# Performance work log

Hardware: AMD Instinct MI355X
Metric: run time of the kernel (lower is better)

The kernel has to match this reference:

```python
import jax, jax.numpy as jnp
import numpy as np

H = 4  # num_heads (hard-coded in module)
RATION = 5


def setup_inputs() -> dict:
    key = jax.random.key(0)
    ks = jax.random.split(key, 14)
    B, T, S, F = 256, 5, 64, 256
    u = 0.05  # keras 'uniform' initializer scale
    d = {}
    d["x"] = jax.random.normal(ks[0], (B, T, S, F), jnp.float32)
    d["atten_bias"] = jax.random.uniform(ks[1], (B, T, S, S), jnp.float32) * 0.1
    d["W_q"] = jax.random.uniform(ks[2], (F, F), jnp.float32, -u, u)
    d["W_v"] = jax.random.uniform(ks[3], (F, F), jnp.float32, -u, u)
    d["W_o"] = jax.random.uniform(ks[4], (F, F), jnp.float32, -u, u)
    d["u_t"] = jax.random.uniform(ks[5], (T,), jnp.float32, -u, u)
    d["dis"] = jax.random.uniform(ks[6], (T, S, S), jnp.float32, -u, u)
    # keep sigma away from 0 to avoid blowing up the Gaussian prior
    d["sigma"] = jax.random.uniform(ks[7], (T, S, 1), jnp.float32, 0.5, 1.0)
    # SE block: fc1 Dense(T*RATION, relu, he_normal), fc2 Dense(T, sigmoid)
    d["fc1_w"] = jax.random.normal(ks[8], (T, T * RATION), jnp.float32) * np.sqrt(2.0 / T).astype(np.float32)
    d["fc1_b"] = jnp.zeros((T * RATION,), jnp.float32)
    d["fc2_w"] = jax.random.normal(ks[9], (T * RATION, T), jnp.float32) * np.sqrt(2.0 / (T * RATION)).astype(np.float32)
    d["fc2_b"] = jnp.zeros((T,), jnp.float32)
    d["bili_w"] = jax.random.uniform(ks[10], (1,), jnp.float32, -u, u)
    return d


def _se_block(o, fc1_w, fc1_b, fc2_w, fc2_b, bili_w):
    # o: [B,T,S,F] -> transpose to [B,S,F,T]; "channel" axis is T
    xt = jnp.transpose(o, (0, 2, 3, 1))
    avg = jnp.mean(xt, axis=(1, 2))  # [B,T]
    mx = jnp.max(xt, axis=(1, 2))    # [B,T]
    se1 = jax.nn.sigmoid(jax.nn.relu(avg @ fc1_w + fc1_b) @ fc2_w + fc2_b)
    se2 = jax.nn.sigmoid(jax.nn.relu(mx @ fc1_w + fc1_b) @ fc2_w + fc2_b)
    w = bili_w  # shape (1,)
    se = (1.0 - w) * se1 + w * se2   # [B,T]
    out = xt * se[:, None, None, :]
    return jnp.transpose(out, (0, 3, 1, 2))  # back to [B,T,S,F]


def reference(x, atten_bias, W_q, W_v, W_o, u_t, dis, sigma, fc1_w, fc1_b, fc2_w, fc2_b, bili_w):
    B, T, S, F = x.shape
    Fh = F // H
    # q, v: project then reshape (row-major split, exactly as TF reshape)
    q = (x @ W_q).reshape(-1, T, S, Fh)          # [H*B, T, S, Fh]
    v = (x @ W_v).reshape(-1, T, S, Fh)          # [H*B, T, S, Fh]
    # k: contract time with u_t, then [B,F,S] -> [H*B, Fh, S]
    k = jnp.einsum('t,btsf->bsf', u_t, x)        # [B, S, F]
    k = jnp.transpose(k, (0, 2, 1)).reshape(-1, Fh, S)  # [H*B, Fh, S]
    score = jnp.einsum('btsf,bfc->btsc', q, k) / jnp.sqrt(jnp.asarray(Fh, x.dtype))
    score = jax.nn.sigmoid(score)                # [H*B, T, S, S]
    score = score - jnp.tile(atten_bias, (H, 1, 1, 1))
    # learned spatial Gaussian prior, broadcast over batch
    prior = (1.0 / (jnp.sqrt(2.0 * jnp.pi) * sigma)) * jnp.exp(-dis ** 2 / (2.0 * sigma ** 2))
    score = score * prior
    # Dropout(0.3) is identity at inference
    score = jnp.sum(score, axis=-2)              # [H*B, T, S]
    atten = v * score[..., None]                 # [H*B, T, S, Fh]
    o = atten.reshape(-1, T, S, F) @ W_o         # [B, T, S, F]
    o = _se_block(o, fc1_w, fc1_b, fc2_w, fc2_b, bili_w)
    return o + x
```

## Files before the change

### kernel.cpp

```cpp
#include <hip/hip_runtime.h>


typedef unsigned short ushort_t;
typedef __attribute__((ext_vector_type(8))) short bf16x8;
typedef __attribute__((ext_vector_type(4))) float f32x4;

__device__ inline ushort_t f2bf(float f) {
  unsigned u = __float_as_uint(f);
  return (ushort_t)((u + 0x7FFFu + ((u >> 16) & 1u)) >> 16);
}
__device__ inline float bflo(unsigned u) { return __uint_as_float(u << 16); }
__device__ inline float bfhi(unsigned u) { return __uint_as_float(u & 0xFFFF0000u); }
__device__ inline uint4 pack8(float4 a, float4 b) {
  uint4 r;
  r.x = (unsigned)f2bf(a.x) | ((unsigned)f2bf(a.y) << 16);
  r.y = (unsigned)f2bf(a.z) | ((unsigned)f2bf(a.w) << 16);
  r.z = (unsigned)f2bf(b.x) | ((unsigned)f2bf(b.y) << 16);
  r.w = (unsigned)f2bf(b.z) | ((unsigned)f2bf(b.w) << 16);
  return r;
}
__device__ inline void gload16(const ushort_t* g, ushort_t* l) {
  __builtin_amdgcn_global_load_lds((const __attribute__((address_space(1))) void*)g,
                                   (__attribute__((address_space(3))) void*)l, 16, 0, 0);
}

__global__ __launch_bounds__(256, 4) void prep_kernel(
    const float* __restrict__ x, const float* __restrict__ u,
    const float* __restrict__ Wq, const float* __restrict__ Wv,
    const float* __restrict__ Wo, const float* __restrict__ dis,
    const float* __restrict__ sigma, const float* __restrict__ bias,
    ushort_t* __restrict__ Wt, float* __restrict__ prior,
    float* __restrict__ bps, ushort_t* __restrict__ kout,
    ushort_t* __restrict__ xb) {
  __shared__ float red[4][64];
  const int blk = blockIdx.x, tid = threadIdx.x;
  if (blk < 768) {
    int id = blk * 256 + tid;
    int mat = id >> 16, rem = id & 65535;
    int n = rem >> 8, k = rem & 255;
    const float* W = mat == 0 ? Wq : (mat == 1 ? Wv : Wo);
    Wt[id] = f2bf(W[k * 256 + n]);
  } else if (blk < 848) {
    int i = (blk - 768) * 256 + tid;
    int ts = i >> 6;
    float sg = sigma[ts];
    float d = dis[i];
    prior[i] = 0.3989422804014327f / sg * __expf(-d * d / (2.f * sg * sg));
  } else if (blk < 2128) {
    int b2 = blk - 848;
    int t = b2 % 5;
    const float* bp = bias + (size_t)b2 * 4096;
    int c = tid & 63, sg_ = tid >> 6;
    float sum = 0.f;
    for (int s = sg_ * 16; s < sg_ * 16 + 16; ++s) {
      float sgm = sigma[t * 64 + s];
      float d = dis[t * 4096 + s * 64 + c];
      float pr = 0.3989422804014327f / sgm * __expf(-d * d / (2.f * sgm * sgm));
      sum += bp[s * 64 + c] * pr;
    }
    red[sg_][c] = sum;
    __syncthreads();
    if (tid < 64)
      bps[(size_t)b2 * 64 + tid] = red[0][tid] + red[1][tid] + red[2][tid] + red[3][tid];
  } else {
    int i = (blk - 2128) * 256 + tid;
    size_t j = (size_t)i * 8;
    int b = (int)(j >> 14);
    int off = (int)(j & 16383);
    const float* xp = x + (size_t)b * 81920 + off;
    ushort_t* xq = xb + (size_t)b * 81920 + off;
    float u0 = u[0], u1 = u[1], u2 = u[2], u3 = u[3], u4 = u[4];
    float4 lo[5], hi[5];
#pragma unroll
    for (int t = 0; t < 5; ++t) {
      lo[t] = *(const float4*)(xp + t * 16384);
      hi[t] = *(const float4*)(xp + t * 16384 + 4);
    }
#pragma unroll
    for (int t = 0; t < 5; ++t)
      *(uint4*)(xq + t * 16384) = pack8(lo[t], hi[t]);
    float4 rl, rh;
    rl.x = u0*lo[0].x + u1*lo[1].x + u2*lo[2].x + u3*lo[3].x + u4*lo[4].x;
    rl.y = u0*lo[0].y + u1*lo[1].y + u2*lo[2].y + u3*lo[3].y + u4*lo[4].y;
    rl.z = u0*lo[0].z + u1*lo[1].z + u2*lo[2].z + u3*lo[3].z + u4*lo[4].z;
    rl.w = u0*lo[0].w + u1*lo[1].w + u2*lo[2].w + u3*lo[3].w + u4*lo[4].w;
    rh.x = u0*hi[0].x + u1*hi[1].x + u2*hi[2].x + u3*hi[3].x + u4*hi[4].x;
    rh.y = u0*hi[0].y + u1*hi[1].y + u2*hi[2].y + u3*hi[3].y + u4*hi[4].y;
    rh.z = u0*hi[0].z + u1*hi[1].z + u2*hi[2].z + u3*hi[3].z + u4*hi[4].z;
    rh.w = u0*hi[0].w + u1*hi[1].w + u2*hi[2].w + u3*hi[3].w + u4*hi[4].w;
    *(uint4*)(kout + j) = pack8(rl, rh);
  }
}

__global__ __launch_bounds__(256) void qscore(const ushort_t* __restrict__ xb,
                                              const ushort_t* __restrict__ Wtq,
                                              const ushort_t* __restrict__ kbuf,
                                              const float* __restrict__ prior,
                                              const float* __restrict__ bps,
                                              float* __restrict__ ssum) {
  __shared__ __align__(16) char smem[46080];
  ushort_t* As_ = (ushort_t*)smem;
  ushort_t* Bs_ = (ushort_t*)(smem + 10240);
  ushort_t* qlds = (ushort_t*)smem;
  const int n = blockIdx.x;
  const int tid = threadIdx.x;
  const int lane = tid & 63, w = tid >> 6;
  const int cl = lane & 15, ql = lane >> 4, l7 = lane & 7;
  const ushort_t* A = xb + (size_t)n * 20480;

  const int c = w * 16 + cl;
  const int nb = n & 255;
  const ushort_t* kbp = kbuf + (size_t)(n >> 2) * 16384 + (n & 3) * 64;
  bf16x8 kfr0 = *(const bf16x8*)(kbp + c * 256 + ql * 8);
  bf16x8 kfr1 = *(const bf16x8*)(kbp + c * 256 + ql * 8 + 32);

  f32x4 acc[5][4];
#pragma unroll
  for (int mi = 0; mi < 5; ++mi)
#pragma unroll
    for (int ni = 0; ni < 4; ++ni) acc[mi][ni] = (f32x4){0.f, 0.f, 0.f, 0.f};

  for (int t4 = 0; t4 < 4; ++t4) {
    const int k0 = t4 * 64;
    if (t4) __syncthreads();
#pragma unroll
    for (int l = 0; l < 3; ++l) {
      int i = l * 256 + tid;
      if (i < 640) {
        int r = i >> 3, cc = i & 7;
        uint4 v = *(const uint4*)(A + (size_t)r * 256 + k0 + cc * 8);
        *(uint4*)&As_[r * 64 + ((cc ^ (r & 7)) * 8)] = v;
      }
    }
#pragma unroll
    for (int l = 0; l < 8; ++l) {
      int i = l * 256 + tid;
      int nn = i >> 3, cc = i & 7;
      uint4 v = *(const uint4*)(Wtq + (size_t)nn * 256 + k0 + cc * 8);
      *(uint4*)&Bs_[nn * 64 + ((cc ^ (nn & 7)) * 8)] = v;
    }
    __syncthreads();
#pragma unroll
    for (int kk = 0; kk < 2; ++kk) {
      const int offk = (((kk << 2) | ql) ^ l7) * 8;
      bf16x8 bfr[4];
#pragma unroll
      for (int ni = 0; ni < 4; ++ni)
        bfr[ni] = *(const bf16x8*)&Bs_[(w * 64 + ni * 16 + cl) * 64 + offk];
#pragma unroll
      for (int mi = 0; mi < 5; ++mi) {
        bf16x8 afr = *(const bf16x8*)&As_[(mi * 16 + cl) * 64 + offk];
#pragma unroll
        for (int ni = 0; ni < 4; ++ni)
          acc[mi][ni] = __builtin_amdgcn_mfma_f32_16x16x32_bf16(afr, bfr[ni], acc[mi][ni], 0, 0, 0);
      }
    }
  }
  __syncthreads();
#pragma unroll
  for (int mi = 0; mi < 5; ++mi)
#pragma unroll
    for (int ni = 0; ni < 4; ++ni)
#pragma unroll
      for (int rr = 0; rr < 4; ++rr)
        qlds[(mi * 64 + 16 * ql + 4 * rr + w) * 72 + ni * 16 + cl] = f2bf(acc[mi][ni][rr]);
  __syncthreads();

#pragma unroll
  for (int t = 0; t < 5; ++t) {
    f32x4 sacc[4];
#pragma unroll
    for (int si = 0; si < 4; ++si) {
      bf16x8 a0 = *(const bf16x8*)&qlds[(t * 64 + si * 16 + cl) * 72 + ql * 8];
      bf16x8 a1 = *(const bf16x8*)&qlds[(t * 64 + si * 16 + cl) * 72 + ql * 8 + 32];
      f32x4 z = (f32x4){0.f, 0.f, 0.f, 0.f};
      z = __builtin_amdgcn_mfma_f32_16x16x32_bf16(a0, kfr0, z, 0, 0, 0);
      z = __builtin_amdgcn_mfma_f32_16x16x32_bf16(a1, kfr1, z, 0, 0, 0);
      sacc[si] = z;
    }
    const float* pp = prior + t * 4096;
    float colsum = 0.f;
#pragma unroll
    for (int si = 0; si < 4; ++si) {
#pragma unroll
      for (int r = 0; r < 4; ++r) {
        int s = si * 16 + ql * 4 + r;
        float sg = 1.f / (1.f + __expf(-sacc[si][r] * 0.125f));
        colsum += sg * pp[s * 64 + c];
      }
    }
    colsum += __shfl_xor(colsum, 16);
    colsum += __shfl_xor(colsum, 32);
    if (ql == 0)
      ssum[(size_t)n * 320 + t * 64 + c] = colsum - bps[((size_t)nb * 5 + t) * 64 + c];
  }
}

template<int SCALE, int SEEPI>
__global__ __launch_bounds__(512, 4) void gemm_mfma(
    const ushort_t* __restrict__ A, const ushort_t* __restrict__ Wt,
    ushort_t* C, const float* __restrict__ ssum,
    float* __restrict__ ravg, float* __restrict__ rmax) {
  __shared__ __align__(16) ushort_t As_[128 * 64];
  __shared__ __align__(16) ushort_t Bs_[256 * 64];
  __shared__ float redS[8], redM[8];
  const int tid = threadIdx.x;
  const int lane = tid & 63;
  const int w = tid >> 6, wr = w >> 2, wc = w & 3;
  const int row0 = blockIdx.x * 128;
  const int cl = lane & 15, ql = lane >> 4, l7 = lane & 7;

  f32x4 acc[4][4];
#pragma unroll
  for (int i = 0; i < 4; ++i)
#pragma unroll
    for (int j = 0; j < 4; ++j) acc[i][j] = (f32x4){0.f, 0.f, 0.f, 0.f};

  for (int t = 0; t < 4; ++t) {
    const int k0 = t * 64;
    if (t) __syncthreads();
#pragma unroll
    for (int l = 0; l < 2; ++l) {
      int i = l * 512 + tid;
      int r = i >> 3, cpos = i & 7, csrc = cpos ^ (r & 7);
      gload16(A + (size_t)(row0 + r) * 256 + k0 + csrc * 8,
              &As_[(l * 512 + w * 64) * 8]);
    }
#pragma unroll
    for (int l = 0; l < 4; ++l) {
      int i = l * 512 + tid;
      int n = i >> 3, cpos = i & 7, csrc = cpos ^ (n & 7);
      gload16(Wt + (size_t)n * 256 + k0 + csrc * 8,
              &Bs_[(l * 512 + w * 64) * 8]);
    }
    __syncthreads();
#pragma unroll
    for (int kk = 0; kk < 2; ++kk) {
      const int offk = (((kk << 2) | ql) ^ l7) * 8;
      bf16x8 bfr[4], afr[4];
#pragma unroll
      for (int ni = 0; ni < 4; ++ni)
        bfr[ni] = *(const bf16x8*)&Bs_[(wc * 64 + ni * 16 + cl) * 64 + offk];
#pragma unroll
      for (int mi = 0; mi < 4; ++mi)
        afr[mi] = *(const bf16x8*)&As_[(wr * 64 + mi * 16 + cl) * 64 + offk];
#pragma unroll
      for (int mi = 0; mi < 4; ++mi)
#pragma unroll
        for (int ni = 0; ni < 4; ++ni)
          acc[mi][ni] = __builtin_amdgcn_mfma_f32_16x16x32_bf16(afr[mi], bfr[ni], acc[mi][ni], 0, 0, 0);
    }
  }
  float lsum = 0.f, lmax = -3.4e38f;
#pragma unroll
  for (int mi = 0; mi < 4; ++mi) {
    float sc[4];
    if (SCALE) {
#pragma unroll
      for (int r = 0; r < 4; ++r)
        sc[r] = ssum[(size_t)(row0 + wr * 64 + mi * 16 + ql * 4 + r) * 4 + wc];
    }
#pragma unroll
    for (int ni = 0; ni < 4; ++ni) {
      int col = wc * 64 + ni * 16 + cl;
      f32x4 v = acc[mi][ni];
#pragma unroll
      for (int r = 0; r < 4; ++r) {
        int row = row0 + wr * 64 + mi * 16 + ql * 4 + r;
        float f = v[r];
        if (SCALE) f *= sc[r];
        C[(size_t)row * 256 + col] = f2bf(f);
        if (SEEPI) { lsum += f; lmax = fmaxf(lmax, f); }
      }
    }
  }
  if (SEEPI) {
#pragma unroll
    for (int off = 32; off; off >>= 1) {
      lsum += __shfl_xor(lsum, off);
      lmax = fmaxf(lmax, __shfl_xor(lmax, off));
    }
    if (lane == 0) { redS[w] = lsum; redM[w] = lmax; }
    __syncthreads();
    if (tid < 2) {
      float s = redS[tid * 4] + redS[tid * 4 + 1] + redS[tid * 4 + 2] + redS[tid * 4 + 3];
      float m = fmaxf(fmaxf(redM[tid * 4], redM[tid * 4 + 1]),
                      fmaxf(redM[tid * 4 + 2], redM[tid * 4 + 3]));
      ravg[blockIdx.x * 2 + tid] = s * (1.f / 16384.f);
      rmax[blockIdx.x * 2 + tid] = m;
    }
  }
}

__global__ __launch_bounds__(256) void final_kernel(
    const ushort_t* __restrict__ xb, const ushort_t* __restrict__ ob,
    const float* __restrict__ ravg, const float* __restrict__ rmax,
    const float* __restrict__ fc1w, const float* __restrict__ fc1b,
    const float* __restrict__ fc2w, const float* __restrict__ fc2b,
    const float* __restrict__ bili, float* __restrict__ out) {
  __shared__ float sse;
  int i = blockIdx.x * 256 + threadIdx.x;
  size_t j = (size_t)i * 4;
  int bt = (int)(j >> 14);
  uint2 uo = *(const uint2*)(ob + j);
  uint2 ux = *(const uint2*)(xb + j);
  if (threadIdx.x == 0) {
    int b = bt / 5, t = bt % 5;
    float avg[5], mx[5];
    for (int tt = 0; tt < 5; ++tt) { avg[tt] = ravg[b * 5 + tt]; mx[tt] = rmax[b * 5 + tt]; }
    float w = bili[0];
    float s12[2];
    for (int p = 0; p < 2; ++p) {
      const float* in = p == 0 ? avg : mx;
      float a = fc2b[t];
      for (int jj = 0; jj < 25; ++jj) {
        float hh = fc1b[jj];
        for (int tt = 0; tt < 5; ++tt) hh += in[tt] * fc1w[tt * 25 + jj];
        a += fmaxf(hh, 0.f) * fc2w[jj * 5 + t];
      }
      s12[p] = 1.f / (1.f + __expf(-a));
    }
    sse = (1.f - w) * s12[0] + w * s12[1];
  }
  __syncthreads();
  float s = sse;
  float4 r = {bflo(uo.x) * s + bflo(ux.x), bfhi(uo.x) * s + bfhi(ux.x),
              bflo(uo.y) * s + bflo(ux.y), bfhi(uo.y) * s + bfhi(ux.y)};
  *(float4*)(out + j) = r;
}

extern "C" void kernel_launch(void* const* d_in, const int* in_sizes, int n_in,
                              void* d_out, int out_size, void* d_ws, size_t ws_size,
                              hipStream_t stream) {
  const float* x     = (const float*)d_in[0];
  const float* bias  = (const float*)d_in[1];
  const float* Wq    = (const float*)d_in[2];
  const float* Wv    = (const float*)d_in[3];
  const float* Wo    = (const float*)d_in[4];
  const float* u_t   = (const float*)d_in[5];
  const float* dis   = (const float*)d_in[6];
  const float* sigma = (const float*)d_in[7];
  const float* fc1w  = (const float*)d_in[8];
  const float* fc1b  = (const float*)d_in[9];
  const float* fc2w  = (const float*)d_in[10];
  const float* fc2b  = (const float*)d_in[11];
  const float* bili  = (const float*)d_in[12];
  float* out = (float*)d_out;

  char* wsb = (char*)d_ws;
  ushort_t* xbuf = (ushort_t*)wsb;             wsb += 41943040;
  ushort_t* qvb  = (ushort_t*)wsb;             wsb += 41943040;
  ushort_t* kb   = (ushort_t*)wsb;             wsb += 8388608;
  ushort_t* Wt   = (ushort_t*)wsb;             wsb += 393216;
  float*    ssum = (float*)wsb;                wsb += 1310720;
  float*    prior= (float*)wsb;                wsb += 81920;
  float*    bps  = (float*)wsb;                wsb += 327680;
  float*    ravg = (float*)wsb;                wsb += 5120;
  float*    rmax = (float*)wsb;                wsb += 5120;

  prep_kernel<<<4176, 256, 0, stream>>>(x, u_t, Wq, Wv, Wo, dis, sigma, bias,
                                        Wt, prior, bps, kb, xbuf);
  qscore<<<1024, 256, 0, stream>>>(xbuf, Wt, kb, prior, bps, ssum);
  gemm_mfma<1, 0><<<640, 512, 0, stream>>>(xbuf, Wt + 65536, qvb, ssum, nullptr, nullptr);
  gemm_mfma<0, 1><<<640, 512, 0, stream>>>(qvb, Wt + 131072, qvb, nullptr, ravg, rmax);
  final_kernel<<<20480, 256, 0, stream>>>(xbuf, qvb, ravg, rmax,
                                          fc1w, fc1b, fc2w, fc2b, bili, out);
}
```

Measured before the change: 154.4 us.

## Fuse V-projection and output-projection GEMMs into one kernel via LDS staging

Replaces the two back-to-back GEMM launches (scaled x@Wv, then @Wo with SE reductions) with a single kernel. Each block computes a 64-row tile of the scaled V projection, keeps it in a swizzled LDS buffer, and immediately multiplies it by Wo. This removes the global write and re-read of the intermediate and one launch. In exchange the tile shrinks from 128 to 64 rows, which lowers per-block MFMA reuse and doubles the weight loads per row, and the extra 32KB of LDS may limit occupancy.

After: 143.4 us. 1.08x faster.

```diff
diff --git a/kernel.cpp b/kernel.cpp
--- a/kernel.cpp
+++ b/kernel.cpp
@@ -196,99 +196,140 @@
   }
 }
 
-template<int SCALE, int SEEPI>
-__global__ __launch_bounds__(512, 4) void gemm_mfma(
-    const ushort_t* __restrict__ A, const ushort_t* __restrict__ Wt,
-    ushort_t* C, const float* __restrict__ ssum,
-    float* __restrict__ ravg, float* __restrict__ rmax) {
-  __shared__ __align__(16) ushort_t As_[128 * 64];
+__global__ __launch_bounds__(512, 4) void vo_gemm(
+    const ushort_t* __restrict__ xb, const ushort_t* __restrict__ Wtv,
+    const ushort_t* __restrict__ Wto, const float* __restrict__ ssum,
+    ushort_t* __restrict__ ob, float* __restrict__ ravg,
+    float* __restrict__ rmax) {
+  __shared__ __align__(16) ushort_t As_[64 * 64];
   __shared__ __align__(16) ushort_t Bs_[256 * 64];
+  __shared__ __align__(16) ushort_t Vs_[64 * 256];
   __shared__ float redS[8], redM[8];
   const int tid = threadIdx.x;
   const int lane = tid & 63;
   const int w = tid >> 6, wr = w >> 2, wc = w & 3;
-  const int row0 = blockIdx.x * 128;
+  const int g = blockIdx.x;
+  const int row0 = g * 64;
   const int cl = lane & 15, ql = lane >> 4, l7 = lane & 7;
 
-  f32x4 acc[4][4];
-#pragma unroll
-  for (int i = 0; i < 4; ++i)
-#pragma unroll
-    for (int j = 0; j < 4; ++j) acc[i][j] = (f32x4){0.f, 0.f, 0.f, 0.f};
+  f32x4 acc[2][4];
+#pragma unroll
+  for (int mi = 0; mi < 2; ++mi)
+#pragma unroll
+    for (int ni = 0; ni < 4; ++ni) acc[mi][ni] = (f32x4){0.f, 0.f, 0.f, 0.f};
 
   for (int t = 0; t < 4; ++t) {
     const int k0 = t * 64;
     if (t) __syncthreads();
-#pragma unroll
-    for (int l = 0; l < 2; ++l) {
-      int i = l * 512 + tid;
+    {
+      int i = tid;
       int r = i >> 3, cpos = i & 7, csrc = cpos ^ (r & 7);
-      gload16(A + (size_t)(row0 + r) * 256 + k0 + csrc * 8,
-              &As_[(l * 512 + w * 64) * 8]);
+      gload16(xb + (size_t)(row0 + r) * 256 + k0 + csrc * 8, &As_[(w * 64) * 8]);
     }
 #pragma unroll
     for (int l = 0; l < 4; ++l) {
       int i = l * 512 + tid;
       int n = i >> 3, cpos = i & 7, csrc = cpos ^ (n & 7);
-      gload16(Wt + (size_t)n * 256 + k0 + csrc * 8,
-              &Bs_[(l * 512 + w * 64) * 8]);
+      gload16(Wtv + (size_t)n * 256 + k0 + csrc * 8, &Bs_[(l * 512 + w * 64) * 8]);
     }
     __syncthreads();
 #pragma unroll
     for (int kk = 0; kk < 2; ++kk) {
       const int offk = (((kk << 2) | ql) ^ l7) * 8;
-      bf16x8 bfr[4], afr[4];
+      bf16x8 bfr[4], afr[2];
 #pragma unroll
       for (int ni = 0; ni < 4; ++ni)
         bfr[ni] = *(const bf16x8*)&Bs_[(wc * 64 + ni * 16 + cl) * 64 + offk];
 #pragma unroll
-      for (int mi = 0; mi < 4; ++mi)
-        afr[mi] = *(const bf16x8*)&As_[(wr * 64 + mi * 16 + cl) * 64 + offk];
-#pragma unroll
-      for (int mi = 0; mi < 4; ++mi)
+      for (int mi = 0; mi < 2; ++mi)
+        afr[mi] = *(const bf16x8*)&As_[(wr * 32 + mi * 16 + cl) * 64 + offk];
+#pragma unroll
+      for (int mi = 0; mi < 2; ++mi)
 #pragma unroll
         for (int ni = 0; ni < 4; ++ni)
           acc[mi][ni] = __builtin_amdgcn_mfma_f32_16x16x32_bf16(afr[mi], bfr[ni], acc[mi][ni], 0, 0, 0);
     }
   }
-  float lsum = 0.f, lmax = -3.4e38f;
-#pragma unroll
-  for (int mi = 0; mi < 4; ++mi) {
+#pragma unroll
+  for (int mi = 0; mi < 2; ++mi) {
     float sc[4];
-    if (SCALE) {
-#pragma unroll
-      for (int r = 0; r < 4; ++r)
-        sc[r] = ssum[(size_t)(row0 + wr * 64 + mi * 16 + ql * 4 + r) * 4 + wc];
-    }
+#pragma unroll
+    for (int r = 0; r < 4; ++r)
+      sc[r] = ssum[(size_t)(row0 + wr * 32 + mi * 16 + ql * 4 + r) * 4 + wc];
 #pragma unroll
     for (int ni = 0; ni < 4; ++ni) {
       int col = wc * 64 + ni * 16 + cl;
-      f32x4 v = acc[mi][ni];
 #pragma unroll
       for (int r = 0; r < 4; ++r) {
-        int row = row0 + wr * 64 + mi * 16 + ql * 4 + r;
-        float f = v[r];
-        if (SCALE) f *= sc[r];
-        C[(size_t)row * 256 + col] = f2bf(f);
-        if (SEEPI) { lsum += f; lmax = fmaxf(lmax, f); }
-      }
-    }
-  }
-  if (SEEPI) {
-#pragma unroll
-    for (int off = 32; off; off >>= 1) {
-      lsum += __shfl_xor(lsum, off);
-      lmax = fmaxf(lmax, __shfl_xor(lmax, off));
-    }
-    if (lane == 0) { redS[w] = lsum; redM[w] = lmax; }
+        int row = wr * 32 + mi * 16 + ql * 4 + r;
+        int ch = (col >> 3) ^ (row & 31);
+        Vs_[row * 256 + ch * 8 + (col & 7)] = f2bf(acc[mi][ni][r] * sc[r]);
+      }
+    }
+  }
+  __syncthreads();
+
+#pragma unroll
+  for (int mi = 0; mi < 2; ++mi)
+#pragma unroll
+    for (int ni = 0; ni < 4; ++ni) acc[mi][ni] = (f32x4){0.f, 0.f, 0.f, 0.f};
+  for (int t = 0; t < 4; ++t) {
+    const int k0 = t * 64;
+    if (t) __syncthreads();
+#pragma unroll
+    for (int l = 0; l < 4; ++l) {
+      int i = l * 512 + tid;
+      int n = i >> 3, cpos = i & 7, csrc = cpos ^ (n & 7);
+      gload16(Wto + (size_t)n * 256 + k0 + csrc * 8, &Bs_[(l * 512 + w * 64) * 8]);
+    }
     __syncthreads();
-    if (tid < 2) {
-      float s = redS[tid * 4] + redS[tid * 4 + 1] + redS[tid * 4 + 2] + redS[tid * 4 + 3];
-      float m = fmaxf(fmaxf(redM[tid * 4], redM[tid * 4 + 1]),
-                      fmaxf(redM[tid * 4 + 2], redM[tid * 4 + 3]));
-      ravg[blockIdx.x * 2 + tid] = s * (1.f / 16384.f);
-      rmax[blockIdx.x * 2 + tid] = m;
-    }
+#pragma unroll
+    for (int kk = 0; kk < 2; ++kk) {
+      const int offk = (((kk << 2) | ql) ^ l7) * 8;
+      const int ch = t * 8 + kk * 4 + ql;
+      bf16x8 bfr[4], afr[2];
+#pragma unroll
+      for (int ni = 0; ni < 4; ++ni)
+        bfr[ni] = *(const bf16x8*)&Bs_[(wc * 64 + ni * 16 + cl) * 64 + offk];
+#pragma unroll
+      for (int mi = 0; mi < 2; ++mi) {
+        int row = wr * 32 + mi * 16 + cl;
+        afr[mi] = *(const bf16x8*)&Vs_[row * 256 + (ch ^ (row & 31)) * 8];
+      }
+#pragma unroll
+      for (int mi = 0; mi < 2; ++mi)
+#pragma unroll
+        for (int ni = 0; ni < 4; ++ni)
+          acc[mi][ni] = __builtin_amdgcn_mfma_f32_16x16x32_bf16(afr[mi], bfr[ni], acc[mi][ni], 0, 0, 0);
+    }
+  }
+  float lsum = 0.f, lmax = -3.4e38f;
+#pragma unroll
+  for (int mi = 0; mi < 2; ++mi)
+#pragma unroll
+    for (int ni = 0; ni < 4; ++ni) {
+      int col = wc * 64 + ni * 16 + cl;
+#pragma unroll
+      for (int r = 0; r < 4; ++r) {
+        int row = row0 + wr * 32 + mi * 16 + ql * 4 + r;
+        float f = acc[mi][ni][r];
+        ob[(size_t)row * 256 + col] = f2bf(f);
+        lsum += f; lmax = fmaxf(lmax, f);
+      }
+    }
+#pragma unroll
+  for (int off = 32; off; off >>= 1) {
+    lsum += __shfl_xor(lsum, off);
+    lmax = fmaxf(lmax, __shfl_xor(lmax, off));
+  }
+  if (lane == 0) { redS[w] = lsum; redM[w] = lmax; }
+  __syncthreads();
+  if (tid == 0) {
+    float s = 0.f, m = -3.4e38f;
+#pragma unroll
+    for (int i = 0; i < 8; ++i) { s += redS[i]; m = fmaxf(m, redM[i]); }
+    ravg[g] = s * (1.f / 16384.f);
+    rmax[g] = m;
   }
 }
 
@@ -361,8 +402,8 @@
   prep_kernel<<<4176, 256, 0, stream>>>(x, u_t, Wq, Wv, Wo, dis, sigma, bias,
                                         Wt, prior, bps, kb, xbuf);
   qscore<<<1024, 256, 0, stream>>>(xbuf, Wt, kb, prior, bps, ssum);
-  gemm_mfma<1, 0><<<640, 512, 0, stream>>>(xbuf, Wt + 65536, qvb, ssum, nullptr, nullptr);
-  gemm_mfma<0, 1><<<640, 512, 0, stream>>>(qvb, Wt + 131072, qvb, nullptr, ravg, rmax);
+  vo_gemm<<<1280, 512, 0, stream>>>(xbuf, Wt + 65536, Wt + 131072, ssum,
+                                    qvb, ravg, rmax);
   final_kernel<<<20480, 256, 0, stream>>>(xbuf, qvb, ravg, rmax,
                                           fc1w, fc1b, fc2w, fc2b, bili, out);
 }
```
